# Optimization experiments

Measured on AMD Instinct MI355X. Metric: run time of the kernel, lower is better.

## Reference

```python
import jax, jax.numpy as jnp
import numpy as np
from jax import lax

DIM = 192
HEADS = 4

def setup_inputs() -> dict:
    key = jax.random.key(0)
    k1, k2, k3, k4 = jax.random.split(key, 4)
    x = jax.random.normal(k1, (8, DIM, 128, 128), dtype=jnp.float32)
    w_qkv = jax.random.normal(k2, (DIM * 3, DIM), dtype=jnp.float32) * 0.05
    w_dw = jax.random.normal(k3, (DIM * 3, 1, 3, 3), dtype=jnp.float32) * 0.1
    w_proj = jax.random.normal(k4, (DIM, DIM), dtype=jnp.float32) * 0.05
    temperature = jnp.ones((HEADS, 1, 1), dtype=jnp.float32)
    return {"x": x, "w_qkv": w_qkv, "w_dw": w_dw, "w_proj": w_proj, "temperature": temperature}

def _l2norm(t, eps=1e-12):
    # F.normalize(t, dim=-1): t / max(||t||_2, eps)
    n = jnp.sqrt(jnp.sum(t * t, axis=-1, keepdims=True))
    return t / jnp.maximum(n, eps)

def reference(x, w_qkv, w_dw, w_proj, temperature):
    b, c, h, w = x.shape
    heads = temperature.shape[0]
    ch = c // heads  # channels per head
    # 1x1 conv (pointwise): dim -> 3*dim
    qkv = jnp.einsum('oi,bihw->bohw', w_qkv, x)
    # 3x3 depthwise conv, groups = 3*dim, padding 1
    qkv = lax.conv_general_dilated(
        qkv, w_dw, window_strides=(1, 1), padding='SAME',
        dimension_numbers=('NCHW', 'OIHW', 'NCHW'),
        feature_group_count=3 * c)
    q, k, v = jnp.split(qkv, 3, axis=1)
    # b (head c) h w -> b head c (h w)
    q = q.reshape(b, heads, ch, h * w)
    k = k.reshape(b, heads, ch, h * w)
    v = v.reshape(b, heads, ch, h * w)
    qn = _l2norm(q)
    kn = _l2norm(k)
    # channel-channel attention: [b, head, ch, ch]
    attn = jnp.einsum('bhcn,bhdn->bhcd', qn, kn) * temperature[None]
    attn = jax.nn.relu(attn)
    out = jnp.einsum('bhcd,bhdn->bhcn', attn, v)
    out = out.reshape(b, c, h, w)
    # output 1x1 projection
    out = jnp.einsum('oi,bihw->bohw', w_proj, out)
    return out
```

## Files before the change

### kernel.cpp

```cpp
#include <hip/hip_runtime.h>

#define BB 8
#define CC 192
#define C3 576
#define HW 16384
#define HEADS 4
#define CHD 48
#define NPLANE (BB*CC)

typedef short s8v __attribute__((ext_vector_type(8)));
typedef float f16v __attribute__((ext_vector_type(16)));
typedef float f4v __attribute__((ext_vector_type(4)));

__device__ __forceinline__ ushort bfu(float f) {
    union { float f; unsigned u; } c; c.f = f;
    unsigned u = c.u + 0x7FFFu + ((c.u >> 16) & 1u);
    return (ushort)(u >> 16);
}
__device__ __forceinline__ float ubf(ushort u) {
    union { unsigned u; float f; } c; c.u = ((unsigned)u) << 16;
    return c.f;
}

__global__ void kw_cvt(const float* __restrict__ w, ushort* __restrict__ wbf) {
    int idx = blockIdx.x * 256 + threadIdx.x;
    if (idx >= C3 * CC) return;
    int o = idx / CC, k = idx % CC;
    int sec = o / CC;
    int ol = o - sec * CC;
    wbf[(size_t)sec * CC * CC + (size_t)(k >> 3) * CC * 8 + ol * 8 + (k & 7)] = bfu(w[idx]);
}

__global__ __launch_bounds__(256) void k_trans(
    const float* __restrict__ xf, ushort* __restrict__ T)
{
    const int b = blockIdx.x, cg = blockIdx.y;
    const int p = blockIdx.z * 1024 + threadIdx.x * 4;
    float a[8][4];
    #pragma unroll
    for (int c = 0; c < 8; c++)
        *(float4*)a[c] = *(const float4*)(xf + ((size_t)(b * CC + cg * 8 + c) * HW + p));
    #pragma unroll
    for (int j = 0; j < 4; j++) {
        unsigned wp[4];
        #pragma unroll
        for (int i = 0; i < 4; i++)
            wp[i] = (unsigned)bfu(a[2*i][j]) | ((unsigned)bfu(a[2*i+1][j]) << 16);
        *(uint4*)(T + ((size_t)(b * 24 + cg) * HW + p + j) * 8) = *(const uint4*)wp;
    }
}

__device__ __forceinline__ void loadk(int ks, const ushort* Ab, const ushort* Bb,
    int kg, int wr, int wc, int ll, int pbase, s8v a[3], s8v b[2])
{
    #pragma unroll
    for (int mt = 0; mt < 3; mt++)
        a[mt] = *(const s8v*)(Ab + ((size_t)(ks * 2 + kg) * CC + wr * 96 + mt * 32 + ll) * 8);
    #pragma unroll
    for (int nt = 0; nt < 2; nt++)
        b[nt] = *(const s8v*)(Bb + ((size_t)(ks * 2 + kg) * HW + pbase + wc * 64 + nt * 32 + ll) * 8);
}

template<int MODE>
__global__ __launch_bounds__(256) void gemm_mfma(
    const ushort* __restrict__ A,
    const ushort* __restrict__ BT,
    ushort* __restrict__ qk, ushort* __restrict__ vpl,
    float* __restrict__ outf)
{
    int lin = blockIdx.x, sec, pt, b;
    if (MODE == 0) {
        int logical = (lin & 7) * 384 + (lin >> 3);
        sec = logical % 3;
        int pb = logical / 3;
        pt = pb & 127; b = pb >> 7;
    } else {
        int logical = (lin & 7) * 128 + (lin >> 3);
        sec = 0; b = logical >> 7; pt = logical & 127;
    }
    const int t = threadIdx.x, lane = t & 63, w = t >> 6;
    const int wr = w >> 1, wc = w & 1;
    const int ll = lane & 31, kg = lane >> 5;
    const int pbase = pt * 128;
    const ushort* Ab = A + (size_t)(MODE == 0 ? sec : b) * CC * CC;
    const ushort* Bb = BT + (size_t)b * 24 * HW * 8;

    f16v acc[3][2];
    #pragma unroll
    for (int mt = 0; mt < 3; mt++)
        #pragma unroll
        for (int nt = 0; nt < 2; nt++)
            #pragma unroll
            for (int i = 0; i < 16; i++) acc[mt][nt][i] = 0.f;

    s8v a0[3], b0[2], a1[3], b1[2];
    loadk(0, Ab, Bb, kg, wr, wc, ll, pbase, a0, b0);
    #pragma unroll
    for (int kk = 0; kk < 6; kk++) {
        loadk(2 * kk + 1, Ab, Bb, kg, wr, wc, ll, pbase, a1, b1);
        #pragma unroll
        for (int mt = 0; mt < 3; mt++)
            #pragma unroll
            for (int nt = 0; nt < 2; nt++)
                acc[mt][nt] = __builtin_amdgcn_mfma_f32_32x32x16_bf16(a0[mt], b0[nt], acc[mt][nt], 0, 0, 0);
        if (kk < 5) loadk(2 * kk + 2, Ab, Bb, kg, wr, wc, ll, pbase, a0, b0);
        #pragma unroll
        for (int mt = 0; mt < 3; mt++)
            #pragma unroll
            for (int nt = 0; nt < 2; nt++)
                acc[mt][nt] = __builtin_amdgcn_mfma_f32_32x32x16_bf16(a1[mt], b1[nt], acc[mt][nt], 0, 0, 0);
    }

    if (MODE == 0) {
        ushort* ob = (sec == 2) ? vpl + (size_t)b * CC * HW
                                : qk + (size_t)(sec * BB + b) * CC * HW;
        #pragma unroll
        for (int mt = 0; mt < 3; mt++)
            #pragma unroll
            for (int nt = 0; nt < 2; nt++)
                #pragma unroll
                for (int r = 0; r < 16; r++) {
                    int o = wr * 96 + mt * 32 + (r & 3) + 8 * (r >> 2) + 4 * kg;
                    int p = pbase + wc * 64 + nt * 32 + ll;
                    ob[(size_t)o * HW + p] = bfu(acc[mt][nt][r]);
                }
    } else {
        #pragma unroll
        for (int mt = 0; mt < 3; mt++)
            #pragma unroll
            for (int nt = 0; nt < 2; nt++)
                #pragma unroll
                for (int r = 0; r < 16; r++) {
                    int o = wr * 96 + mt * 32 + (r & 3) + 8 * (r >> 2) + 4 * kg;
                    int p = pbase + wc * 64 + nt * 32 + ll;
                    outf[((size_t)b * CC + o) * HW + p] = acc[mt][nt][r];
                }
    }
}

__global__ __launch_bounds__(256) void k_dw_bf(
    ushort* __restrict__ qk,
    const float* __restrict__ wdw, float* __restrict__ sq, float* __restrict__ sk)
{
    __shared__ ushort rows[10][128];
    __shared__ float red[4];
    int pid = blockIdx.x;
    int sec = pid / NPLANE, rem = pid % NPLANE;
    int b = rem / CC, c = rem % CC;
    ushort* p = qk + ((size_t)(sec * BB + b) * CC + c) * HW;
    const float* wc9 = wdw + (size_t)(sec * CC + c) * 9;
    float w0=wc9[0],w1=wc9[1],w2=wc9[2],w3=wc9[3],w4=wc9[4],w5=wc9[5],w6=wc9[6],w7=wc9[7],w8=wc9[8];
    const int t = threadIdx.x, lr = t >> 5, lx = (t & 31) * 4;
    float ss = 0.f;
    if (t < 32) ((ushort4*)rows[0])[t] = ((const ushort4*)p)[t];
    __syncthreads();
    for (int y0 = 0; y0 < 128; y0 += 8) {
        int ry = y0 + 1 + lr;
        if (ry < 128) *(ushort4*)&rows[ry % 10][lx] = *(const ushort4*)(p + (size_t)ry * 128 + lx);
        __syncthreads();
        const int oy = y0 + lr;
        float a0=0,a1=0,a2=0,a3=0;
        if (oy >= 1) {
            const ushort* rw = rows[(oy - 1) % 10];
            float m0=ubf(rw[lx]),m1=ubf(rw[lx+1]),m2=ubf(rw[lx+2]),m3=ubf(rw[lx+3]);
            float lf = lx ? ubf(rw[lx-1]) : 0.f, rt = (lx < 124) ? ubf(rw[lx+4]) : 0.f;
            a0 += w0*lf + w1*m0 + w2*m1;  a1 += w0*m0 + w1*m1 + w2*m2;
            a2 += w0*m1 + w1*m2 + w2*m3;  a3 += w0*m2 + w1*m3 + w2*rt;
        }
        {
            const ushort* rw = rows[oy % 10];
            float m0=ubf(rw[lx]),m1=ubf(rw[lx+1]),m2=ubf(rw[lx+2]),m3=ubf(rw[lx+3]);
            float lf = lx ? ubf(rw[lx-1]) : 0.f, rt = (lx < 124) ? ubf(rw[lx+4]) : 0.f;
            a0 += w3*lf + w4*m0 + w5*m1;  a1 += w3*m0 + w4*m1 + w5*m2;
            a2 += w3*m1 + w4*m2 + w5*m3;  a3 += w3*m2 + w4*m3 + w5*rt;
        }
        if (oy + 1 < 128) {
            const ushort* rw = rows[(oy + 1) % 10];
            float m0=ubf(rw[lx]),m1=ubf(rw[lx+1]),m2=ubf(rw[lx+2]),m3=ubf(rw[lx+3]);
            float lf = lx ? ubf(rw[lx-1]) : 0.f, rt = (lx < 124) ? ubf(rw[lx+4]) : 0.f;
            a0 += w6*lf + w7*m0 + w8*m1;  a1 += w6*m0 + w7*m1 + w8*m2;
            a2 += w6*m1 + w7*m2 + w8*m3;  a3 += w6*m2 + w7*m3 + w8*rt;
        }
        ss += a0*a0 + a1*a1 + a2*a2 + a3*a3;
        __syncthreads();
        ushort4 o4; o4.x = bfu(a0); o4.y = bfu(a1); o4.z = bfu(a2); o4.w = bfu(a3);
        *(ushort4*)(p + (size_t)oy * 128 + lx) = o4;
    }
    for (int off = 32; off; off >>= 1) ss += __shfl_down(ss, off);
    if ((t & 63) == 0) red[t >> 6] = ss;
    __syncthreads();
    if (t == 0) (sec == 0 ? sq : sk)[b * CC + c] = red[0] + red[1] + red[2] + red[3];
}

__global__ __launch_bounds__(256) void k_dw_v(
    const ushort* __restrict__ vb, const float* __restrict__ wdw,
    ushort* __restrict__ vT)
{
    __shared__ ushort obuf[4][8][128];
    const int cg = blockIdx.x, b = blockIdx.y, yq = blockIdx.z;
    const int t = threadIdx.x;
    const int c = t >> 5, lr = (t >> 3) & 3, xo = t & 7;
    const int ch = cg * 8 + c;
    const ushort* p = vb + ((size_t)b * CC + ch) * HW;
    const float* wc9 = wdw + (size_t)(2 * CC + ch) * 9;
    float wt[9];
    #pragma unroll
    for (int i = 0; i < 9; i++) wt[i] = wc9[i];
    ushort* tb = vT + (size_t)(b * 24 + cg) * HW * 8;
    const int x0 = xo * 16;

    for (int ic = 0; ic < 8; ic++) {
        const int y = yq * 32 + ic * 4 + lr;
        float a[16];
        #pragma unroll
        for (int j = 0; j < 16; j++) a[j] = 0.f;
        #pragma unroll
        for (int dy = 0; dy < 3; dy++) {
            int ry = y - 1 + dy;
            if (ry >= 0 && ry < 128) {
                const ushort* r = p + (size_t)ry * 128 + x0;
                float wv[18];
                uint4 v0 = *(const uint4*)r;
                uint4 v1 = *(const uint4*)(r + 8);
                unsigned uu[8] = {v0.x, v0.y, v0.z, v0.w, v1.x, v1.y, v1.z, v1.w};
                #pragma unroll
                for (int q = 0; q < 8; q++) {
                    union { unsigned u; float f; } lo, hi;
                    lo.u = uu[q] << 16;  hi.u = uu[q] & 0xFFFF0000u;
                    wv[1 + 2*q] = lo.f;  wv[2 + 2*q] = hi.f;
                }
                wv[0]  = x0 ? ubf(r[-1]) : 0.f;
                wv[17] = (x0 < 112) ? ubf(r[16]) : 0.f;
                float t0 = wt[dy*3], t1 = wt[dy*3+1], t2 = wt[dy*3+2];
                #pragma unroll
                for (int j = 0; j < 16; j++)
                    a[j] += t0 * wv[j] + t1 * wv[j+1] + t2 * wv[j+2];
            }
        }
        __syncthreads();
        ushort tmp[16];
        #pragma unroll
        for (int j = 0; j < 16; j++) tmp[j] = bfu(a[j]);
        *(int4*)&obuf[lr][c][x0]     = *(int4*)&tmp[0];
        *(int4*)&obuf[lr][c][x0 + 8] = *(int4*)&tmp[8];
        __syncthreads();
        #pragma unroll
        for (int rep = 0; rep < 2; rep++) {
            int u = t + rep * 256;
            int row = u >> 7, x = u & 127;
            int4 gi;
            ushort* g = (ushort*)&gi;
            #pragma unroll
            for (int cc = 0; cc < 8; cc++) g[cc] = obuf[row][cc][x];
            int yg = yq * 32 + ic * 4 + row;
            *(int4*)(tb + ((size_t)yg * 128 + x) * 8) = gi;
        }
    }
}

__global__ __launch_bounds__(256) void k_gram(
    const ushort* __restrict__ qk, float* __restrict__ G)
{
    int slab = blockIdx.x, h = blockIdx.y, b = blockIdx.z;
    const int t = threadIdx.x, lane = t & 63, w = t >> 6;
    const ushort* qb = qk + ((size_t)b * CC + h * CHD) * HW;
    const ushort* kb = qk + ((size_t)(BB + b) * CC + h * CHD) * HW;
    const int ll = lane & 15, lh = lane >> 4;
    f4v acc[3][3];
    #pragma unroll
    for (int i = 0; i < 3; i++)
        #pragma unroll
        for (int j = 0; j < 3; j++)
            #pragma unroll
            for (int r = 0; r < 4; r++) acc[i][j][r] = 0.f;
    const int nbase = slab * 512 + w * 128 + lh * 8;
    #pragma unroll
    for (int s = 0; s < 4; s++) {
        const int n = nbase + s * 32;
        s8v aq[3], bk[3];
        #pragma unroll
        for (int mt = 0; mt < 3; mt++)
            aq[mt] = *(const s8v*)(qb + (size_t)(mt * 16 + ll) * HW + n);
        #pragma unroll
        for (int mt = 0; mt < 3; mt++)
            bk[mt] = *(const s8v*)(kb + (size_t)(mt * 16 + ll) * HW + n);
        #pragma unroll
        for (int i = 0; i < 3; i++)
            #pragma unroll
            for (int j = 0; j < 3; j++)
                acc[i][j] = __builtin_amdgcn_mfma_f32_16x16x32_bf16(aq[i], bk[j], acc[i][j], 0, 0, 0);
    }
    float* Gb = G + (size_t)(b * HEADS + h) * CHD * CHD;
    #pragma unroll
    for (int i = 0; i < 3; i++)
        #pragma unroll
        for (int j = 0; j < 3; j++)
            #pragma unroll
            for (int r = 0; r < 4; r++) {
                int cc = i * 16 + lh * 4 + r, d = j * 16 + ll;
                atomicAdd(&Gb[cc * CHD + d], acc[i][j][r]);
            }
}

__global__ __launch_bounds__(256) void k_compose(
    const float* __restrict__ G, const float* __restrict__ sq, const float* __restrict__ sk,
    const float* __restrict__ temp, const float* __restrict__ wproj,
    ushort* __restrict__ Mbf)
{
    __shared__ float attnS[CHD * CHD];
    __shared__ float wS[CC * CHD];
    int h = blockIdx.x, b = blockIdx.y, t = threadIdx.x;
    float tv = temp[h];
    const float* Gb = G + (size_t)(b * HEADS + h) * CHD * CHD;
    const float* sqb = sq + b * CC + h * CHD;
    const float* skb = sk + b * CC + h * CHD;
    #pragma unroll
    for (int i = 0; i < 9; i++) {
        int idx = i * 256 + t;
        int c = idx / CHD, d = idx % CHD;
        float nq = fmaxf(sqrtf(sqb[c]), 1e-12f);
        float nk = fmaxf(sqrtf(skb[d]), 1e-12f);
        float v = Gb[idx] * tv / (nq * nk);
        attnS[idx] = fmaxf(v, 0.f);
    }
    #pragma unroll
    for (int i = 0; i < 36; i++) {
        int idx = i * 256 + t;
        wS[idx] = wproj[(idx / CHD) * CC + h * CHD + idx % CHD];
    }
    __syncthreads();
    ushort* Mb = Mbf + (size_t)b * CC * CC;
    #pragma unroll
    for (int i = 0; i < 36; i++) {
        int idx = i * 256 + t;
        int o = idx / CHD, d = idx % CHD;
        float s = 0.f;
        #pragma unroll 8
        for (int c2 = 0; c2 < CHD; c2++)
            s += wS[o * CHD + c2] * attnS[c2 * CHD + d];
        int cglob = h * CHD + d;
        Mb[(size_t)(cglob >> 3) * CC * 8 + o * 8 + (cglob & 7)] = bfu(s);
    }
}

extern "C" void kernel_launch(void* const* d_in, const int* in_sizes, int n_in,
                              void* d_out, int out_size, void* d_ws, size_t ws_size,
                              hipStream_t stream)
{
    const float* x      = (const float*)d_in[0];
    const float* w_qkv  = (const float*)d_in[1];
    const float* w_dw   = (const float*)d_in[2];
    const float* w_proj = (const float*)d_in[3];
    const float* temp   = (const float*)d_in[4];
    float* out = (float*)d_out;

    ushort* qk = (ushort*)d_out;

    ushort* xT = (ushort*)d_ws;
    ushort* vb = xT + (size_t)BB * CC * HW;
    float*  G  = (float*)(vb + (size_t)BB * CC * HW);
    float*  sq = G + (size_t)BB * HEADS * CHD * CHD;
    float*  sk = sq + (size_t)BB * CC;
    ushort* wbf = (ushort*)(sk + (size_t)BB * CC);
    ushort* Mbf = wbf + (size_t)C3 * CC;

    kw_cvt<<<dim3((C3 * CC + 255) / 256), 256, 0, stream>>>(w_qkv, wbf);
    hipMemsetAsync(G, 0, (size_t)BB * HEADS * CHD * CHD * sizeof(float), stream);

    k_trans<<<dim3(BB, 24, 16), 256, 0, stream>>>(x, xT);

    gemm_mfma<0><<<dim3(3072), 256, 0, stream>>>(wbf, xT, qk, vb, nullptr);

    k_dw_bf<<<dim3(2 * NPLANE), 256, 0, stream>>>(qk, w_dw, sq, sk);

    k_dw_v<<<dim3(24, BB, 4), 256, 0, stream>>>(vb, w_dw, xT);

    k_gram<<<dim3(32, HEADS, BB), 256, 0, stream>>>(qk, G);

    k_compose<<<dim3(HEADS, BB), 256, 0, stream>>>(G, sq, sk, temp, w_proj, Mbf);

    gemm_mfma<1><<<dim3(1024), 256, 0, stream>>>(Mbf, xT, nullptr, nullptr, out);
}
```

Measured before the change: 398.4 us.

## Fold weight conversion and Gram zeroing into transpose; stage GEMM stores through LDS

Removes the separate weight-conversion kernel and the memset by having a few k_trans blocks zero G and convert w_qkv, which saves two launches. Both GEMM epilogues now write each accumulator tile into a per-wave LDS patch and then issue 16-byte row-contiguous global stores, replacing scattered 2- and 4-byte stores. The depthwise q/k kernel now handles 16 rows per iteration with an 18-row ring, which halves the number of barriers, and it packs outputs with v_cvt_pk_bf16_f32. In exchange, the GEMM uses extra LDS, and the depthwise kernel's bf16 rounding now comes from the hardware conversion instruction instead of the software routine.

```diff
diff --git a/kernel.cpp b/kernel.cpp
--- a/kernel.cpp
+++ b/kernel.cpp
@@ -22,20 +22,30 @@
     return c.f;
 }
 
-__global__ void kw_cvt(const float* __restrict__ w, ushort* __restrict__ wbf) {
-    int idx = blockIdx.x * 256 + threadIdx.x;
-    if (idx >= C3 * CC) return;
-    int o = idx / CC, k = idx % CC;
-    int sec = o / CC;
-    int ol = o - sec * CC;
-    wbf[(size_t)sec * CC * CC + (size_t)(k >> 3) * CC * 8 + ol * 8 + (k & 7)] = bfu(w[idx]);
-}
-
 __global__ __launch_bounds__(256) void k_trans(
-    const float* __restrict__ xf, ushort* __restrict__ T)
+    const float* __restrict__ xf, ushort* __restrict__ T,
+    const float* __restrict__ wq, ushort* __restrict__ wbf, float* __restrict__ G)
 {
     const int b = blockIdx.x, cg = blockIdx.y;
     const int p = blockIdx.z * 1024 + threadIdx.x * 4;
+    if (blockIdx.z == 0) {
+        if (cg == 0) {
+            float4 z = {0.f, 0.f, 0.f, 0.f};
+            int base = b * 9216 + threadIdx.x * 4;
+            #pragma unroll
+            for (int i = 0; i < 9; i++) *(float4*)(G + base + i * 1024) = z;
+        } else if (cg == 1) {
+            int base = b * 13824;
+            #pragma unroll 2
+            for (int i = 0; i < 54; i++) {
+                int idx = base + i * 256 + threadIdx.x;
+                int o = idx / CC, k = idx % CC;
+                int sec = o / CC;
+                int ol = o - sec * CC;
+                wbf[(size_t)sec * CC * CC + (size_t)(k >> 3) * CC * 8 + ol * 8 + (k & 7)] = bfu(wq[idx]);
+            }
+        }
+    }
     float a[8][4];
     #pragma unroll
     for (int c = 0; c < 8; c++)
@@ -68,6 +78,8 @@
     ushort* __restrict__ qk, ushort* __restrict__ vpl,
     float* __restrict__ outf)
 {
+    __shared__ ushort RepU[MODE == 0 ? 4 * 32 * 40 : 4];
+    __shared__ float  RepF[MODE == 1 ? 4 * 32 * 36 : 4];
     int lin = blockIdx.x, sec, pt, b;
     if (MODE == 0) {
         int logical = (lin & 7) * 384 + (lin >> 3);
@@ -112,29 +124,47 @@
     }
 
     if (MODE == 0) {
+        ushort* patch = RepU + w * (32 * 40);
         ushort* ob = (sec == 2) ? vpl + (size_t)b * CC * HW
                                 : qk + (size_t)(sec * BB + b) * CC * HW;
         #pragma unroll
         for (int mt = 0; mt < 3; mt++)
             #pragma unroll
-            for (int nt = 0; nt < 2; nt++)
-                #pragma unroll
-                for (int r = 0; r < 16; r++) {
-                    int o = wr * 96 + mt * 32 + (r & 3) + 8 * (r >> 2) + 4 * kg;
-                    int p = pbase + wc * 64 + nt * 32 + ll;
-                    ob[(size_t)o * HW + p] = bfu(acc[mt][nt][r]);
+            for (int nt = 0; nt < 2; nt++) {
+                #pragma unroll
+                for (int g = 0; g < 4; g++)
+                    #pragma unroll
+                    for (int j = 0; j < 4; j++)
+                        patch[(j + 8 * g + 4 * kg) * 40 + ll] = bfu(acc[mt][nt][4 * g + j]);
+                #pragma unroll
+                for (int i = 0; i < 2; i++) {
+                    int c = lane + 64 * i;
+                    int ol = c >> 2, p8 = (c & 3) * 8;
+                    int4 v = *(const int4*)&patch[ol * 40 + p8];
+                    int o = wr * 96 + mt * 32 + ol;
+                    *(int4*)(ob + (size_t)o * HW + pbase + wc * 64 + nt * 32 + p8) = v;
                 }
+            }
     } else {
-        #pragma unroll
-        for (int mt = 0; mt < 3; mt++)
-            #pragma unroll
-            for (int nt = 0; nt < 2; nt++)
-                #pragma unroll
-                for (int r = 0; r < 16; r++) {
-                    int o = wr * 96 + mt * 32 + (r & 3) + 8 * (r >> 2) + 4 * kg;
-                    int p = pbase + wc * 64 + nt * 32 + ll;
-                    outf[((size_t)b * CC + o) * HW + p] = acc[mt][nt][r];
+        float* patch = RepF + w * (32 * 36);
+        #pragma unroll
+        for (int mt = 0; mt < 3; mt++)
+            #pragma unroll
+            for (int nt = 0; nt < 2; nt++) {
+                #pragma unroll
+                for (int g = 0; g < 4; g++)
+                    #pragma unroll
+                    for (int j = 0; j < 4; j++)
+                        patch[(j + 8 * g + 4 * kg) * 36 + ll] = acc[mt][nt][4 * g + j];
+                #pragma unroll
+                for (int i = 0; i < 4; i++) {
+                    int c = lane + 64 * i;
+                    int ol = c >> 3, p4 = (c & 7) * 4;
+                    float4 v = *(const float4*)&patch[ol * 36 + p4];
+                    int o = wr * 96 + mt * 32 + ol;
+                    *(float4*)(outf + ((size_t)b * CC + o) * HW + pbase + wc * 64 + nt * 32 + p4) = v;
                 }
+            }
     }
 }
 
@@ -142,7 +172,7 @@
     ushort* __restrict__ qk,
     const float* __restrict__ wdw, float* __restrict__ sq, float* __restrict__ sk)
 {
-    __shared__ ushort rows[10][128];
+    __shared__ ushort rows[18][128];
     __shared__ float red[4];
     int pid = blockIdx.x;
     int sec = pid / NPLANE, rem = pid % NPLANE;
@@ -154,37 +184,46 @@
     float ss = 0.f;
     if (t < 32) ((ushort4*)rows[0])[t] = ((const ushort4*)p)[t];
     __syncthreads();
-    for (int y0 = 0; y0 < 128; y0 += 8) {
-        int ry = y0 + 1 + lr;
-        if (ry < 128) *(ushort4*)&rows[ry % 10][lx] = *(const ushort4*)(p + (size_t)ry * 128 + lx);
+    for (int y0 = 0; y0 < 128; y0 += 16) {
+        int ry1 = y0 + 1 + lr, ry2 = y0 + 9 + lr;
+        if (ry1 < 128) *(ushort4*)&rows[ry1 % 18][lx] = *(const ushort4*)(p + (size_t)ry1 * 128 + lx);
+        if (ry2 < 128) *(ushort4*)&rows[ry2 % 18][lx] = *(const ushort4*)(p + (size_t)ry2 * 128 + lx);
         __syncthreads();
-        const int oy = y0 + lr;
-        float a0=0,a1=0,a2=0,a3=0;
-        if (oy >= 1) {
-            const ushort* rw = rows[(oy - 1) % 10];
-            float m0=ubf(rw[lx]),m1=ubf(rw[lx+1]),m2=ubf(rw[lx+2]),m3=ubf(rw[lx+3]);
-            float lf = lx ? ubf(rw[lx-1]) : 0.f, rt = (lx < 124) ? ubf(rw[lx+4]) : 0.f;
-            a0 += w0*lf + w1*m0 + w2*m1;  a1 += w0*m0 + w1*m1 + w2*m2;
-            a2 += w0*m1 + w1*m2 + w2*m3;  a3 += w0*m2 + w1*m3 + w2*rt;
+        uint2 outv[2];
+        #pragma unroll
+        for (int half = 0; half < 2; half++) {
+            const int oy = y0 + half * 8 + lr;
+            float a0=0,a1=0,a2=0,a3=0;
+            if (oy >= 1) {
+                const ushort* rw = rows[(oy - 1) % 18];
+                float m0=ubf(rw[lx]),m1=ubf(rw[lx+1]),m2=ubf(rw[lx+2]),m3=ubf(rw[lx+3]);
+                float lf = lx ? ubf(rw[lx-1]) : 0.f, rt = (lx < 124) ? ubf(rw[lx+4]) : 0.f;
+                a0 += w0*lf + w1*m0 + w2*m1;  a1 += w0*m0 + w1*m1 + w2*m2;
+                a2 += w0*m1 + w1*m2 + w2*m3;  a3 += w0*m2 + w1*m3 + w2*rt;
+            }
+            {
+                const ushort* rw = rows[oy % 18];
+                float m0=ubf(rw[lx]),m1=ubf(rw[lx+1]),m2=ubf(rw[lx+2]),m3=ubf(rw[lx+3]);
+                float lf = lx ? ubf(rw[lx-1]) : 0.f, rt = (lx < 124) ? ubf(rw[lx+4]) : 0.f;
+                a0 += w3*lf + w4*m0 + w5*m1;  a1 += w3*m0 + w4*m1 + w5*m2;
+                a2 += w3*m1 + w4*m2 + w5*m3;  a3 += w3*m2 + w4*m3 + w5*rt;
+            }
+            if (oy + 1 < 128) {
+                const ushort* rw = rows[(oy + 1) % 18];
+                float m0=ubf(rw[lx]),m1=ubf(rw[lx+1]),m2=ubf(rw[lx+2]),m3=ubf(rw[lx+3]);
+                float lf = lx ? ubf(rw[lx-1]) : 0.f, rt = (lx < 124) ? ubf(rw[lx+4]) : 0.f;
+                a0 += w6*lf + w7*m0 + w8*m1;  a1 += w6*m0 + w7*m1 + w8*m2;
+                a2 += w6*m1 + w7*m2 + w8*m3;  a3 += w6*m2 + w7*m3 + w8*rt;
+            }
+            ss += a0*a0 + a1*a1 + a2*a2 + a3*a3;
+            unsigned r01, r23;
+            asm("v_cvt_pk_bf16_f32 %0, %1, %2" : "=v"(r01) : "v"(a0), "v"(a1));
+            asm("v_cvt_pk_bf16_f32 %0, %1, %2" : "=v"(r23) : "v"(a2), "v"(a3));
+            outv[half].x = r01; outv[half].y = r23;
         }
-        {
-            const ushort* rw = rows[oy % 10];
-            float m0=ubf(rw[lx]),m1=ubf(rw[lx+1]),m2=ubf(rw[lx+2]),m3=ubf(rw[lx+3]);
-            float lf = lx ? ubf(rw[lx-1]) : 0.f, rt = (lx < 124) ? ubf(rw[lx+4]) : 0.f;
-            a0 += w3*lf + w4*m0 + w5*m1;  a1 += w3*m0 + w4*m1 + w5*m2;
-            a2 += w3*m1 + w4*m2 + w5*m3;  a3 += w3*m2 + w4*m3 + w5*rt;
-        }
-        if (oy + 1 < 128) {
-            const ushort* rw = rows[(oy + 1) % 10];
-            float m0=ubf(rw[lx]),m1=ubf(rw[lx+1]),m2=ubf(rw[lx+2]),m3=ubf(rw[lx+3]);
-            float lf = lx ? ubf(rw[lx-1]) : 0.f, rt = (lx < 124) ? ubf(rw[lx+4]) : 0.f;
-            a0 += w6*lf + w7*m0 + w8*m1;  a1 += w6*m0 + w7*m1 + w8*m2;
-            a2 += w6*m1 + w7*m2 + w8*m3;  a3 += w6*m2 + w7*m3 + w8*rt;
-        }
-        ss += a0*a0 + a1*a1 + a2*a2 + a3*a3;
         __syncthreads();
-        ushort4 o4; o4.x = bfu(a0); o4.y = bfu(a1); o4.z = bfu(a2); o4.w = bfu(a3);
-        *(ushort4*)(p + (size_t)oy * 128 + lx) = o4;
+        *(uint2*)(p + (size_t)(y0 + lr) * 128 + lx) = outv[0];
+        *(uint2*)(p + (size_t)(y0 + 8 + lr) * 128 + lx) = outv[1];
     }
     for (int off = 32; off; off >>= 1) ss += __shfl_down(ss, off);
     if ((t & 63) == 0) red[t >> 6] = ss;
@@ -364,10 +403,7 @@
     ushort* wbf = (ushort*)(sk + (size_t)BB * CC);
     ushort* Mbf = wbf + (size_t)C3 * CC;
 
-    kw_cvt<<<dim3((C3 * CC + 255) / 256), 256, 0, stream>>>(w_qkv, wbf);
-    hipMemsetAsync(G, 0, (size_t)BB * HEADS * CHD * CHD * sizeof(float), stream);
-
-    k_trans<<<dim3(BB, 24, 16), 256, 0, stream>>>(x, xT);
+    k_trans<<<dim3(BB, 24, 16), 256, 0, stream>>>(x, xT, w_qkv, wbf, G);
 
     gemm_mfma<0><<<dim3(3072), 256, 0, stream>>>(wbf, xT, qk, vb, nullptr);
 
```

After: 402.9 us. No clear change (+1.1%).
